# Kernel optimization log

Measured on AMD Instinct MI355X. Metric: run time of the kernel, lower is better.

The kernel has to match this reference:

```python
import jax, jax.numpy as jnp
import numpy as np

S, T, B = 32, 64, 64          # sentences, tokens/sentence, batch
V, E, H, G, C = 32000, 128, 128, 128, 5  # vocab, embed, intra hid, inter hid, classes


def _gru_dir(x, h0, Wih, Whh, bih, bhh):
    # x: [T,B,D]; Wih: [3H,D]; Whh: [3H,H]  (PyTorch GRU gate order r,z,n)
    xg = jnp.einsum('tbd,gd->tbg', x, Wih) + bih  # precompute input gates [T,B,3H]
    def step(h, xt):
        gh = h @ Whh.T + bhh
        ir, iz, inn = jnp.split(xt, 3, axis=-1)
        hr, hz, hn = jnp.split(gh, 3, axis=-1)
        r = jax.nn.sigmoid(ir + hr)
        z = jax.nn.sigmoid(iz + hz)
        n = jnp.tanh(inn + r * hn)
        hnew = (1 - z) * n + z * h
        return hnew, hnew
    _, out = jax.lax.scan(step, h0, xg)
    return out  # [T,B,H]


def _bigru(x, Wih, Whh, bih, bhh):
    # x: [T,B,D]; Wih: [2,3H,D] (fwd, bwd). Zero initial state (init_hidden()).
    h0 = jnp.zeros((x.shape[1], Whh.shape[-1]), x.dtype)
    of = _gru_dir(x, h0, Wih[0], Whh[0], bih[0], bhh[0])
    ob = _gru_dir(x[::-1], h0, Wih[1], Whh[1], bih[1], bhh[1])[::-1]
    return jnp.concatenate([of, ob], axis=-1)  # [T,B,2H]


def setup_inputs() -> dict:
    key = jax.random.key(0)
    ks = iter(jax.random.split(key, 20))
    u = lambda k, shp, s: jax.random.uniform(k, shp, jnp.float32, -s, s)
    tokens = jax.random.randint(next(ks), (S, T, B), 0, V)
    return {
        'tokens': tokens,
        'embed_table': jax.random.normal(next(ks), (V, E), jnp.float32),
        # intra biGRU (input E, hidden H)
        'Wih_intra': u(next(ks), (2, 3 * H, E), 0.08),
        'Whh_intra': u(next(ks), (2, 3 * H, H), 0.08),
        'bih_intra': u(next(ks), (2, 3 * H), 0.08),
        'bhh_intra': u(next(ks), (2, 3 * H), 0.08),
        # intra attention
        'W_W_intra': u(next(ks), (2 * H, 2 * H), 0.1),
        'b_intra': u(next(ks), (2 * H,), 0.1),
        'proj_intra': u(next(ks), (2 * H,), 0.1),
        # inter biGRU (input 2H, hidden G)
        'Wih_inter': u(next(ks), (2, 3 * G, 2 * H), 0.08),
        'Whh_inter': u(next(ks), (2, 3 * G, G), 0.08),
        'bih_inter': u(next(ks), (2, 3 * G), 0.08),
        'bhh_inter': u(next(ks), (2, 3 * G), 0.08),
        # inter attention
        'W_W_inter': u(next(ks), (2 * G, 2 * G), 0.1),
        'b_inter': u(next(ks), (2 * G,), 0.1),
        'proj_inter': u(next(ks), (2 * G,), 0.1),
        # final linear
        'W_final': u(next(ks), (C, 2 * G), 0.06),
        'b_final': u(next(ks), (C,), 0.06),
    }


def reference(tokens, embed_table, Wih_intra, Whh_intra, bih_intra, bhh_intra,
              W_W_intra, b_intra, proj_intra, Wih_inter, Whh_inter, bih_inter,
              bhh_inter, W_W_inter, b_inter, proj_inter, W_final, b_final):
    # ---- intra (word-level) per sentence, fresh zero state each sentence ----
    emb = embed_table[tokens]                                   # [S,T,B,E]
    intra_out = jax.vmap(
        lambda xs: _bigru(xs, Wih_intra, Whh_intra, bih_intra, bhh_intra)
    )(emb)                                                      # [S,T,B,2H]
    u1 = jnp.tanh(jnp.einsum('stbh,hk->stbk', intra_out, W_W_intra) + b_intra)
    a1 = jnp.einsum('stbk,k->stb', u1, proj_intra)              # [S,T,B]
    a1 = jax.nn.softmax(a1, axis=1)                             # softmax over tokens
    sent_vecs = jnp.einsum('stb,stbh->sbh', a1, intra_out)      # [S,B,2H]
    # ---- inter (sentence-level) ----
    inter_out = _bigru(sent_vecs, Wih_inter, Whh_inter, bih_inter, bhh_inter)  # [S,B,2G]
    u2 = jnp.tanh(jnp.einsum('sbh,hk->sbk', inter_out, W_W_inter) + b_inter)
    a2 = jnp.einsum('sbk,k->sb', u2, proj_inter)                # NO softmax (faithful to source)
    doc_vec = jnp.einsum('sb,sbh->bh', a2, inter_out)           # [B,2G]
    final_map = doc_vec @ W_final.T + b_final                   # [B,C]
    return final_map
```

## Files before the change

kernel.cpp:

```cpp
#include <hip/hip_runtime.h>

#define S_ 32
#define T_ 64
#define B_ 64
#define V_ 32000
#define E_ 128
#define H_ 128
#define G_ 128
#define C_ 5

typedef short s8v __attribute__((ext_vector_type(8)));
typedef __bf16 b8v __attribute__((ext_vector_type(8)));
typedef float f32x4 __attribute__((ext_vector_type(4)));

template <typename V>
__device__ inline auto mfma_sel(V a, V b, f32x4 c, int)
    -> decltype(__builtin_amdgcn_mfma_f32_16x16x32_bf16(a, b, c, 0, 0, 0)) {
  return __builtin_amdgcn_mfma_f32_16x16x32_bf16(a, b, c, 0, 0, 0);
}
template <typename V>
__device__ inline f32x4 mfma_sel(V a, V b, f32x4 c, long) {
  return __builtin_amdgcn_mfma_f32_16x16x32_bf16(
      __builtin_bit_cast(b8v, a), __builtin_bit_cast(b8v, b), c, 0, 0, 0);
}
__device__ inline f32x4 mfma16(s8v a, s8v b, f32x4 c) { return mfma_sel(a, b, c, 0); }

__device__ inline float b2f(unsigned short u) {
  union { unsigned int i; float f; } v; v.i = ((unsigned int)u) << 16; return v.f;
}
__device__ inline unsigned short f2b(float f) {
  union { float f; unsigned int i; } v; v.f = f;
  return (unsigned short)((v.i + 0x8000u) >> 16);
}
__device__ inline unsigned short f2b_rne(float f) {
  union { float f; unsigned int i; } v; v.f = f;
  unsigned int r = (v.i + 0x7fffu + ((v.i >> 16) & 1u)) >> 16;
  return (unsigned short)r;
}
__device__ inline s8v cvt8(const float* p) {
  const float4 a = *(const float4*)p;
  const float4 b = *(const float4*)(p + 4);
  s8v r;
  r[0] = (short)f2b_rne(a.x); r[1] = (short)f2b_rne(a.y);
  r[2] = (short)f2b_rne(a.z); r[3] = (short)f2b_rne(a.w);
  r[4] = (short)f2b_rne(b.x); r[5] = (short)f2b_rne(b.y);
  r[6] = (short)f2b_rne(b.z); r[7] = (short)f2b_rne(b.w);
  return r;
}
__device__ inline float fsigm(float x) {
  return __builtin_amdgcn_rcpf(1.f + __builtin_amdgcn_exp2f(-1.44269504f * x));
}
__device__ inline float ftanh(float x) {
  return 1.f - 2.f * __builtin_amdgcn_rcpf(1.f + __builtin_amdgcn_exp2f(2.88539008f * x));
}

__device__ inline void lds_barrier() {
  asm volatile("s_waitcnt lgkmcnt(0)\n\ts_barrier" ::: "memory");
}

__global__ __launch_bounds__(256) void k_gtab(
    const float* __restrict__ emb,
    const float* __restrict__ wih,
    const float* __restrict__ bih,
    const float* __restrict__ bhh,
    const float* __restrict__ wwi,
    unsigned short* __restrict__ gtab,
    unsigned short* __restrict__ wta)
{
  __shared__ __align__(16) unsigned short smem[64 * 264];
  const int bid = blockIdx.x, tid = threadIdx.x;
  if (bid >= 500) {
    const int n0 = (bid - 500) * 64;
    for (int i = 0; i < 64; ++i) {
      int cid = i * 256 + tid;
      int k = cid >> 6, nl = cid & 63;
      smem[nl * 264 + k] = f2b_rne(wwi[k * 256 + n0 + nl]);
    }
    __syncthreads();
    for (int i = 0; i < 8; ++i) {
      int cid = i * 256 + tid;
      int nl = cid >> 5, k8 = cid & 31;
      *(int4*)&wta[(size_t)(n0 + nl) * 256 + k8 * 8] =
          *(const int4*)&smem[nl * 264 + k8 * 8];
    }
    return;
  }
  const int vbase = bid * 64;
  for (int i = 0; i < 8; ++i) {
    int cid = i * 256 + tid;
    int row = cid >> 5, kc = cid & 31;
    float4 v = *(const float4*)&emb[(size_t)(vbase + row) * 128 + kc * 4];
    ushort4 u;
    u.x = f2b_rne(v.x); u.y = f2b_rne(v.y); u.z = f2b_rne(v.z); u.w = f2b_rne(v.w);
    *(ushort4*)&smem[row * 136 + kc * 4] = u;
  }
  __syncthreads();
  const int w = tid >> 6, l = tid & 63, q = l >> 4, ln = l & 15;
  s8v af[4][4];
  for (int mt = 0; mt < 4; ++mt)
    for (int kf = 0; kf < 4; ++kf)
      af[mt][kf] = *(const s8v*)&smem[(mt * 16 + ln) * 136 + kf * 32 + q * 8];
  for (int nchunk = 0; nchunk < 6; ++nchunk) {
    const int nbase = nchunk * 128;
    s8v bf[2][4];
    float bias[2];
    for (int nt = 0; nt < 2; ++nt) {
      int c = nbase + (w * 2 + nt) * 16 + ln;
      int g = (c < 384) ? c : (c - 384);
      bias[nt] = bih[c] + (g < 256 ? bhh[c] : 0.f);
      for (int kf = 0; kf < 4; ++kf)
        bf[nt][kf] = cvt8(&wih[(size_t)c * 128 + kf * 32 + q * 8]);
    }
    for (int mt = 0; mt < 4; ++mt) {
      for (int nt = 0; nt < 2; ++nt) {
        f32x4 acc = {0.f, 0.f, 0.f, 0.f};
        for (int kf = 0; kf < 4; ++kf) acc = mfma16(af[mt][kf], bf[nt][kf], acc);
        const int col = nbase + (w * 2 + nt) * 16 + ln;
        for (int r = 0; r < 4; ++r) {
          const int row = vbase + mt * 16 + q * 4 + r;
          gtab[(size_t)row * 768 + col] = f2b_rne(acc[r] + bias[nt]);
        }
      }
    }
  }
}

__global__ __launch_bounds__(512) void k_intra(
    const int* __restrict__ tokens,
    const unsigned short* __restrict__ gtab,
    const float* __restrict__ whh,
    const float* __restrict__ bhh,
    unsigned short* __restrict__ iout)
{
  const int bid = blockIdx.x;
  const int s = bid >> 3, dir = (bid >> 2) & 1, bq = bid & 3;
  const int bbase = bq * 16;
  const int tid = threadIdx.x;
  const int w = tid >> 6, l = tid & 63, q = l >> 4, ln = l & 15;
  const int gbase = w * 16, g0 = gbase + q * 4;

  __shared__ __align__(16) unsigned short hb[2][16 * 136];
  __shared__ int tokl[T_ * 16];

  for (int i = tid; i < 2 * 16 * 136; i += 512) ((unsigned short*)hb)[i] = 0;
  for (int i = tid; i < T_ * 16; i += 512) {
    int t = i >> 4, bl = i & 15;
    tokl[i] = tokens[(s * T_ + t) * B_ + bbase + bl];
  }

  s8v af[3][4];
  float hbn[4];
  const float* whd = whh + (size_t)dir * (384 * 128);
  const float* bhd = bhh + dir * 384;
  for (int g3 = 0; g3 < 3; ++g3) {
    const int R = g3 * 128 + gbase;
    for (int kf = 0; kf < 4; ++kf)
      af[g3][kf] = cvt8(&whd[(size_t)(R + ln) * 128 + kf * 32 + q * 8]);
  }
  for (int r = 0; r < 4; ++r) hbn[r] = bhd[256 + gbase + q * 4 + r];
  float h[4] = {0.f, 0.f, 0.f, 0.f};
  const int b = bbase + ln;
  __syncthreads();

  ushort4 Xr[4], Xz[4], Xn[4];
#define GLOAD_I(slot, st)                                                   \
  do {                                                                      \
    int tt_ = (st) > (T_ - 1) ? (T_ - 1) : (st);                            \
    int tg_ = dir ? (T_ - 1 - tt_) : tt_;                                   \
    const unsigned short* gp_ =                                             \
        gtab + (size_t)tokl[tg_ * 16 + ln] * 768 + dir * 384 + g0;          \
    Xr[slot] = *(const ushort4*)&gp_[0];                                    \
    Xz[slot] = *(const ushort4*)&gp_[128];                                  \
    Xn[slot] = *(const ushort4*)&gp_[256];                                  \
  } while (0)

  GLOAD_I(0, 0);
  GLOAD_I(1, 1);

  int p = 0;
  for (int it = 0; it < T_ / 4; ++it) {
#pragma unroll
    for (int j = 0; j < 4; ++j) {
      const int step = it * 4 + j;
      const int t = dir ? (T_ - 1 - step) : step;
      GLOAD_I((j + 2) & 3, step + 2);

      s8v bfr[4];
      for (int kf = 0; kf < 4; ++kf)
        bfr[kf] = *(const s8v*)&hb[p][ln * 136 + kf * 32 + q * 8];
      f32x4 c0 = {0.f, 0.f, 0.f, 0.f}, c1 = c0, c2 = c0;
      for (int kf = 0; kf < 4; ++kf) {
        c0 = mfma16(af[0][kf], bfr[kf], c0);
        c1 = mfma16(af[1][kf], bfr[kf], c1);
        c2 = mfma16(af[2][kf], bfr[kf], c2);
      }

      const unsigned short* xrp = (const unsigned short*)&Xr[j];
      const unsigned short* xzp = (const unsigned short*)&Xz[j];
      const unsigned short* xnp = (const unsigned short*)&Xn[j];
      unsigned short hnb[4];
      for (int r = 0; r < 4; ++r) {
        float rr = fsigm(b2f(xrp[r]) + c0[r]);
        float zz = fsigm(b2f(xzp[r]) + c1[r]);
        float nn = ftanh(b2f(xnp[r]) + rr * (c2[r] + hbn[r]));
        float hv = zz * (h[r] - nn) + nn;
        h[r] = hv;
        hnb[r] = f2b(hv);
      }
      ushort4 hv4; hv4.x = hnb[0]; hv4.y = hnb[1]; hv4.z = hnb[2]; hv4.w = hnb[3];
      *(ushort4*)&hb[p ^ 1][ln * 136 + g0] = hv4;
      *(ushort4*)&iout[((size_t)(s * T_ + t) * B_ + b) * 256 + dir * 128 + g0] = hv4;
      lds_barrier();
      p ^= 1;
    }
  }
#undef GLOAD_I
}

__global__ __launch_bounds__(512, 1) void k_attn(
    const unsigned short* __restrict__ iout,
    const unsigned short* __restrict__ wta,
    const float* __restrict__ bint,
    const float* __restrict__ proj,
    float* __restrict__ sv)
{
  __shared__ __align__(16) unsigned short wlds[256 * 256];
  __shared__ float lgbuf[8][16];
  __shared__ float lbuf[8][8];
  const int tid = threadIdx.x, bid = blockIdx.x;
  const int s = bid >> 3, b0 = (bid & 7) * 8;
  for (int i = 0; i < 16; ++i) {
    int cid = i * 512 + tid;
    int n = cid >> 5, kc = cid & 31;
    *(int4*)&wlds[n * 256 + ((kc ^ (n & 15)) << 3)] =
        *(const int4*)&wta[(size_t)n * 256 + kc * 8];
  }
  const int w = tid >> 6, l = tid & 63, q = l >> 4, ln = l & 15;
  float bbv[16], ppv[16];
  for (int nt = 0; nt < 16; ++nt) {
    bbv[nt] = bint[nt * 16 + ln];
    ppv[nt] = proj[nt * 16 + ln];
  }
  __syncthreads();

  float O[8][8];
  for (int kf = 0; kf < 8; ++kf)
    for (int j = 0; j < 8; ++j) O[kf][j] = 0.f;
  float l_acc = 0.f;

  for (int tile = 0; tile < 4; ++tile) {
    const int t = (w * 4 + tile) * 2 + (ln >> 3);
    const size_t row = (size_t)((s * T_ + t) * B_ + b0 + (ln & 7));
    s8v af[8];
    for (int kf = 0; kf < 8; ++kf)
      af[kf] = *(const s8v*)&iout[row * 256 + kf * 32 + q * 8];
    float p0 = 0.f, p1 = 0.f, p2 = 0.f, p3 = 0.f;
    for (int nt = 0; nt < 16; ++nt) {
      f32x4 c = {0.f, 0.f, 0.f, 0.f};
      for (int kf = 0; kf < 8; ++kf) {
        s8v bf = *(const s8v*)&wlds[(nt * 16 + ln) * 256 + (((kf * 4 + q) ^ ln) << 3)];
        c = mfma16(af[kf], bf, c);
      }
      p0 += ppv[nt] * ftanh(c[0] + bbv[nt]);
      p1 += ppv[nt] * ftanh(c[1] + bbv[nt]);
      p2 += ppv[nt] * ftanh(c[2] + bbv[nt]);
      p3 += ppv[nt] * ftanh(c[3] + bbv[nt]);
    }
    for (int d = 1; d < 16; d <<= 1) {
      p0 += __shfl_xor(p0, d); p1 += __shfl_xor(p1, d);
      p2 += __shfl_xor(p2, d); p3 += __shfl_xor(p3, d);
    }
    if (ln == 0) {
      lgbuf[w][q * 4 + 0] = p0; lgbuf[w][q * 4 + 1] = p1;
      lgbuf[w][q * 4 + 2] = p2; lgbuf[w][q * 4 + 3] = p3;
    }
    const float lg = lgbuf[w][ln];
    const float e = __builtin_amdgcn_exp2f(1.44269504f * lg);
    l_acc += e;
    for (int kf = 0; kf < 8; ++kf)
      for (int j = 0; j < 8; ++j)
        O[kf][j] += e * b2f((unsigned short)af[kf][j]);
  }
  l_acc += __shfl_xor(l_acc, 8);
  for (int kf = 0; kf < 8; ++kf)
    for (int j = 0; j < 8; ++j) O[kf][j] += __shfl_xor(O[kf][j], 8);
  __syncthreads();
  float* obuf = (float*)wlds;
  if (ln < 8) {
    const int base = w * 2048 + ln * 256 + q * 8;
    for (int kf = 0; kf < 8; ++kf) {
      float4 v0; v0.x = O[kf][0]; v0.y = O[kf][1]; v0.z = O[kf][2]; v0.w = O[kf][3];
      float4 v1; v1.x = O[kf][4]; v1.y = O[kf][5]; v1.z = O[kf][6]; v1.w = O[kf][7];
      *(float4*)&obuf[base + kf * 32]     = v0;
      *(float4*)&obuf[base + kf * 32 + 4] = v1;
    }
    if (q == 0) lbuf[w][ln] = l_acc;
  }
  __syncthreads();
  const int idx = tid * 4;
  const int bb_ = idx >> 8;
  float4 acc; acc.x = 0.f; acc.y = 0.f; acc.z = 0.f; acc.w = 0.f;
  float lsum = 0.f;
  for (int w8 = 0; w8 < 8; ++w8) {
    const float4 v = *(const float4*)&obuf[w8 * 2048 + idx];
    acc.x += v.x; acc.y += v.y; acc.z += v.z; acc.w += v.w;
    lsum += lbuf[w8][bb_];
  }
  const float inv = __builtin_amdgcn_rcpf(lsum);
  float4 r; r.x = acc.x * inv; r.y = acc.y * inv; r.z = acc.z * inv; r.w = acc.w * inv;
  *(float4*)&sv[(size_t)((s * B_ + b0 + bb_) * 256) + (idx & 255)] = r;
}

__global__ __launch_bounds__(256) void k_xgi(
    const float* __restrict__ sv,
    const float* __restrict__ wihI,
    const float* __restrict__ bihI,
    const float* __restrict__ bhhI,
    float* __restrict__ xgi)
{
  const int bid = blockIdx.x, tid = threadIdx.x;
  const int r0 = bid * 8;
  __shared__ float svl[8 * 256];
  for (int i = 0; i < 8; ++i) svl[i * 256 + tid] = sv[(size_t)(r0 + i) * 256 + tid];
  __syncthreads();
  for (int cc = 0; cc < 3; ++cc) {
    const int c = cc * 256 + tid;
    const int dir = c / 384, g = c - dir * 384;
    const float bias = bihI[c] + (g < 256 ? bhhI[c] : 0.f);
    float acc[8];
    for (int i = 0; i < 8; ++i) acc[i] = bias;
    const float* wr = wihI + (size_t)c * 256;
    for (int hh = 0; hh < 256; ++hh) {
      const float wv = wr[hh];
      for (int i = 0; i < 8; ++i) acc[i] += wv * svl[i * 256 + hh];
    }
    for (int i = 0; i < 8; ++i)
      xgi[((size_t)dir * 2048 + r0 + i) * 384 + g] = acc[i];
  }
}

__global__ __launch_bounds__(512) void k_inter(
    const float* __restrict__ xgi,
    const float* __restrict__ whh,
    const float* __restrict__ bhh,
    float* __restrict__ io2)
{
  const int bid = blockIdx.x;
  const int dir = bid >> 2, bq = bid & 3, bbase = bq * 16;
  const int tid = threadIdx.x;
  const int w = tid >> 6, l = tid & 63, q = l >> 4, ln = l & 15;
  const int gbase = w * 16, g0 = gbase + q * 4;
  __shared__ __align__(16) unsigned short hb[2][16 * 136];
  for (int i = tid; i < 2 * 16 * 136; i += 512) ((unsigned short*)hb)[i] = 0;
  s8v af[3][4];
  float hbn[4];
  const float* whd = whh + (size_t)dir * (384 * 128);
  const float* bhd = bhh + dir * 384;
  for (int g3 = 0; g3 < 3; ++g3) {
    const int R = g3 * 128 + gbase;
    for (int kf = 0; kf < 4; ++kf)
      af[g3][kf] = cvt8(&whd[(size_t)(R + ln) * 128 + kf * 32 + q * 8]);
  }
  for (int r = 0; r < 4; ++r) hbn[r] = bhd[256 + gbase + q * 4 + r];
  float h[4] = {0.f, 0.f, 0.f, 0.f};
  const int b = bbase + ln;
  __syncthreads();

  float4 Vr[4], Vz[4], Vn[4];
#define GLOAD_S(slot, st)                                                   \
  do {                                                                      \
    int tt_ = (st) > (S_ - 1) ? (S_ - 1) : (st);                            \
    int sg_ = dir ? (S_ - 1 - tt_) : tt_;                                   \
    const float* xp_ = xgi + ((size_t)dir * 2048 + sg_ * 64 + b) * 384 + g0;\
    Vr[slot] = *(const float4*)&xp_[0];                                     \
    Vz[slot] = *(const float4*)&xp_[128];                                   \
    Vn[slot] = *(const float4*)&xp_[256];                                   \
  } while (0)

  GLOAD_S(0, 0);
  GLOAD_S(1, 1);

  int p = 0;
  for (int it = 0; it < S_ / 4; ++it) {
#pragma unroll
    for (int j = 0; j < 4; ++j) {
      const int step = it * 4 + j;
      const int sI = dir ? (S_ - 1 - step) : step;
      GLOAD_S((j + 2) & 3, step + 2);

      s8v bfr[4];
      for (int kf = 0; kf < 4; ++kf)
        bfr[kf] = *(const s8v*)&hb[p][ln * 136 + kf * 32 + q * 8];
      f32x4 c0 = {0.f, 0.f, 0.f, 0.f}, c1 = c0, c2 = c0;
      for (int kf = 0; kf < 4; ++kf) {
        c0 = mfma16(af[0][kf], bfr[kf], c0);
        c1 = mfma16(af[1][kf], bfr[kf], c1);
        c2 = mfma16(af[2][kf], bfr[kf], c2);
      }
      const float irv[4] = {Vr[j].x, Vr[j].y, Vr[j].z, Vr[j].w};
      const float izv[4] = {Vz[j].x, Vz[j].y, Vz[j].z, Vz[j].w};
      const float inv[4] = {Vn[j].x, Vn[j].y, Vn[j].z, Vn[j].w};
      unsigned short hnb[4];
      for (int r = 0; r < 4; ++r) {
        float rr = fsigm(irv[r] + c0[r]);
        float zz = fsigm(izv[r] + c1[r]);
        float nn = ftanh(inv[r] + rr * (c2[r] + hbn[r]));
        float hv = zz * (h[r] - nn) + nn;
        h[r] = hv;
        hnb[r] = f2b(hv);
      }
      ushort4 hv4; hv4.x = hnb[0]; hv4.y = hnb[1]; hv4.z = hnb[2]; hv4.w = hnb[3];
      *(ushort4*)&hb[p ^ 1][ln * 136 + g0] = hv4;
      float4 of4; of4.x = h[0]; of4.y = h[1]; of4.z = h[2]; of4.w = h[3];
      *(float4*)&io2[((size_t)(sI * 64 + b)) * 256 + dir * 128 + g0] = of4;
      lds_barrier();
      p ^= 1;
    }
  }
#undef GLOAD_S
}

__global__ __launch_bounds__(256) void k_attn_i(
    const float* __restrict__ io2,
    const float* __restrict__ wwI,
    const float* __restrict__ bI,
    const float* __restrict__ projI,
    float* __restrict__ a2)
{
  const int bid = blockIdx.x, tid = threadIdx.x;
  const int r0 = bid * 8;
  __shared__ float iol[8 * 256];
  __shared__ float red[4 * 8];
  for (int i = 0; i < 8; ++i) iol[i * 256 + tid] = io2[(size_t)(r0 + i) * 256 + tid];
  __syncthreads();
  float acc[8];
  for (int i = 0; i < 8; ++i) acc[i] = 0.f;
  for (int hh = 0; hh < 256; ++hh) {
    const float wv = wwI[hh * 256 + tid];
    for (int i = 0; i < 8; ++i) acc[i] += wv * iol[i * 256 + hh];
  }
  const float bb = bI[tid], pp = projI[tid];
  float p[8];
  for (int i = 0; i < 8; ++i) p[i] = pp * ftanh(acc[i] + bb);
  for (int d = 1; d < 64; d <<= 1)
    for (int i = 0; i < 8; ++i) p[i] += __shfl_xor(p[i], d);
  const int w = tid >> 6, l = tid & 63;
  if (l == 0)
    for (int i = 0; i < 8; ++i) red[w * 8 + i] = p[i];
  __syncthreads();
  if (tid < 8) a2[r0 + tid] = red[tid] + red[8 + tid] + red[16 + tid] + red[24 + tid];
}

__global__ __launch_bounds__(256) void k_final(
    const float* __restrict__ a2,
    const float* __restrict__ io2,
    const float* __restrict__ wf,
    const float* __restrict__ bfi,
    float* __restrict__ out)
{
  const int b = blockIdx.x, tid = threadIdx.x;
  __shared__ float av[S_];
  __shared__ float dv[256];
  __shared__ float red[4];
  if (tid < S_) av[tid] = a2[tid * 64 + b];
  __syncthreads();
  float acc = 0.f;
  for (int s = 0; s < S_; ++s) acc += av[s] * io2[((size_t)(s * 64 + b)) * 256 + tid];
  dv[tid] = acc;
  __syncthreads();
  for (int c = 0; c < C_; ++c) {
    float pv = wf[c * 256 + tid] * dv[tid];
    for (int d = 1; d < 64; d <<= 1) pv += __shfl_xor(pv, d);
    const int w = tid >> 6, l = tid & 63;
    if (l == 0) red[w] = pv;
    __syncthreads();
    if (tid == 0)
      out[b * C_ + c] = red[0] + red[1] + red[2] + red[3] + bfi[c];
    __syncthreads();
  }
}

extern "C" void kernel_launch(void* const* d_in, const int* in_sizes, int n_in,
                              void* d_out, int out_size, void* d_ws, size_t ws_size,
                              hipStream_t stream) {
  (void)in_sizes; (void)n_in; (void)out_size; (void)ws_size;
  const int*   tokens = (const int*)d_in[0];
  const float* emb    = (const float*)d_in[1];
  const float* wih_a  = (const float*)d_in[2];
  const float* whh_a  = (const float*)d_in[3];
  const float* bih_a  = (const float*)d_in[4];
  const float* bhh_a  = (const float*)d_in[5];
  const float* ww_a   = (const float*)d_in[6];
  const float* b_a    = (const float*)d_in[7];
  const float* proj_a = (const float*)d_in[8];
  const float* wih_i  = (const float*)d_in[9];
  const float* whh_i  = (const float*)d_in[10];
  const float* bih_i  = (const float*)d_in[11];
  const float* bhh_i  = (const float*)d_in[12];
  const float* ww_i   = (const float*)d_in[13];
  const float* b_i    = (const float*)d_in[14];
  const float* proj_i = (const float*)d_in[15];
  const float* w_fin  = (const float*)d_in[16];
  const float* b_fin  = (const float*)d_in[17];

  char* ws = (char*)d_ws;
  unsigned short* gtab = (unsigned short*)(ws + 0);
  unsigned short* wta  = (unsigned short*)(ws + 49152000);
  unsigned short* iout = (unsigned short*)(ws + 49283072);
  float* sv  = (float*)(ws + 117440512);
  float* xgi = (float*)(ws + 119537664);
  float* io2 = (float*)(ws + 125829120);
  float* a2  = (float*)(ws + 127926272);

  k_gtab<<<504, 256, 0, stream>>>(emb, wih_a, bih_a, bhh_a, ww_a, gtab, wta);
  k_intra<<<256, 512, 0, stream>>>(tokens, gtab, whh_a, bhh_a, iout);
  k_attn<<<256, 512, 0, stream>>>(iout, wta, b_a, proj_a, sv);
  k_xgi<<<256, 256, 0, stream>>>(sv, wih_i, bih_i, bhh_i, xgi);
  k_inter<<<8, 512, 0, stream>>>(xgi, whh_i, bhh_i, io2);
  k_attn_i<<<256, 256, 0, stream>>>(io2, ww_i, b_i, proj_i, a2);
  k_final<<<64, 256, 0, stream>>>(a2, io2, w_fin, b_fin, (float*)d_out);
}
```

Before: 311.8 us.

## Fuse inter-GRU input projection into intra attention via bf16 MFMA, deepen prefetch

Removes the separate k_xgi kernel. The intra attention kernel now writes its sentence vectors as bf16 to LDS and computes the inter-GRU input gate projection there with MFMA, using a bf16 copy of Wih_inter that k_gtab now also produces. This drops one launch, the fp32 sv round trip through global memory and the scalar FMA GEMM, at the cost of bf16 rounding on the sentence vectors and the weights. The token row offset is also precomputed in LDS, and the GRU gate prefetch distance goes from two steps to three in both recurrent kernels, which adds register pressure.

```diff
diff --git a/kernel.cpp b/kernel.cpp
--- a/kernel.cpp
+++ b/kernel.cpp
@@ -64,11 +64,24 @@
     const float* __restrict__ bih,
     const float* __restrict__ bhh,
     const float* __restrict__ wwi,
+    const float* __restrict__ wihI,
     unsigned short* __restrict__ gtab,
-    unsigned short* __restrict__ wta)
+    unsigned short* __restrict__ wta,
+    unsigned short* __restrict__ wib)
 {
   __shared__ __align__(16) unsigned short smem[64 * 264];
   const int bid = blockIdx.x, tid = threadIdx.x;
+  if (bid >= 504) {
+    const int cb = bid - 504;
+    for (int i = 0; i < 48; ++i) {
+      int e4 = cb * 12288 + i * 256 + tid;
+      float4 v = *(const float4*)&wihI[(size_t)e4 * 4];
+      ushort4 u;
+      u.x = f2b_rne(v.x); u.y = f2b_rne(v.y); u.z = f2b_rne(v.z); u.w = f2b_rne(v.w);
+      *(ushort4*)&wib[(size_t)e4 * 4] = u;
+    }
+    return;
+  }
   if (bid >= 500) {
     const int n0 = (bid - 500) * 64;
     for (int i = 0; i < 64; ++i) {
@@ -145,7 +158,7 @@
   for (int i = tid; i < 2 * 16 * 136; i += 512) ((unsigned short*)hb)[i] = 0;
   for (int i = tid; i < T_ * 16; i += 512) {
     int t = i >> 4, bl = i & 15;
-    tokl[i] = tokens[(s * T_ + t) * B_ + bbase + bl];
+    tokl[i] = tokens[(s * T_ + t) * B_ + bbase + bl] * 768 + dir * 384;
   }
 
   s8v af[3][4];
@@ -168,7 +181,7 @@
     int tt_ = (st) > (T_ - 1) ? (T_ - 1) : (st);                            \
     int tg_ = dir ? (T_ - 1 - tt_) : tt_;                                   \
     const unsigned short* gp_ =                                             \
-        gtab + (size_t)tokl[tg_ * 16 + ln] * 768 + dir * 384 + g0;          \
+        gtab + (size_t)(tokl[tg_ * 16 + ln] + g0);                          \
     Xr[slot] = *(const ushort4*)&gp_[0];                                    \
     Xz[slot] = *(const ushort4*)&gp_[128];                                  \
     Xn[slot] = *(const ushort4*)&gp_[256];                                  \
@@ -176,6 +189,7 @@
 
   GLOAD_I(0, 0);
   GLOAD_I(1, 1);
+  GLOAD_I(2, 2);
 
   int p = 0;
   for (int it = 0; it < T_ / 4; ++it) {
@@ -183,7 +197,7 @@
     for (int j = 0; j < 4; ++j) {
       const int step = it * 4 + j;
       const int t = dir ? (T_ - 1 - step) : step;
-      GLOAD_I((j + 2) & 3, step + 2);
+      GLOAD_I((j + 3) & 3, step + 3);
 
       s8v bfr[4];
       for (int kf = 0; kf < 4; ++kf)
@@ -222,7 +236,10 @@
     const unsigned short* __restrict__ wta,
     const float* __restrict__ bint,
     const float* __restrict__ proj,
-    float* __restrict__ sv)
+    const unsigned short* __restrict__ wib,
+    const float* __restrict__ bihI,
+    const float* __restrict__ bhhI,
+    float* __restrict__ xgi)
 {
   __shared__ __align__(16) unsigned short wlds[256 * 256];
   __shared__ float lgbuf[8][16];
@@ -286,6 +303,7 @@
     for (int j = 0; j < 8; ++j) O[kf][j] += __shfl_xor(O[kf][j], 8);
   __syncthreads();
   float* obuf = (float*)wlds;
+  unsigned short* svl = (unsigned short*)(((char*)wlds) + 65536);
   if (ln < 8) {
     const int base = w * 2048 + ln * 256 + q * 8;
     for (int kf = 0; kf < 8; ++kf) {
@@ -295,6 +313,11 @@
       *(float4*)&obuf[base + kf * 32 + 4] = v1;
     }
     if (q == 0) lbuf[w][ln] = l_acc;
+  }
+  {
+    ushort4 z4; z4.x = 0; z4.y = 0; z4.z = 0; z4.w = 0;
+    int rr = 8 + (tid >> 6), cc = (tid & 63) * 4;
+    *(ushort4*)&svl[rr * 264 + cc] = z4;
   }
   __syncthreads();
   const int idx = tid * 4;
@@ -307,35 +330,30 @@
     lsum += lbuf[w8][bb_];
   }
   const float inv = __builtin_amdgcn_rcpf(lsum);
-  float4 r; r.x = acc.x * inv; r.y = acc.y * inv; r.z = acc.z * inv; r.w = acc.w * inv;
-  *(float4*)&sv[(size_t)((s * B_ + b0 + bb_) * 256) + (idx & 255)] = r;
-}
-
-__global__ __launch_bounds__(256) void k_xgi(
-    const float* __restrict__ sv,
-    const float* __restrict__ wihI,
-    const float* __restrict__ bihI,
-    const float* __restrict__ bhhI,
-    float* __restrict__ xgi)
-{
-  const int bid = blockIdx.x, tid = threadIdx.x;
-  const int r0 = bid * 8;
-  __shared__ float svl[8 * 256];
-  for (int i = 0; i < 8; ++i) svl[i * 256 + tid] = sv[(size_t)(r0 + i) * 256 + tid];
-  __syncthreads();
-  for (int cc = 0; cc < 3; ++cc) {
-    const int c = cc * 256 + tid;
-    const int dir = c / 384, g = c - dir * 384;
-    const float bias = bihI[c] + (g < 256 ? bhhI[c] : 0.f);
-    float acc[8];
-    for (int i = 0; i < 8; ++i) acc[i] = bias;
-    const float* wr = wihI + (size_t)c * 256;
-    for (int hh = 0; hh < 256; ++hh) {
-      const float wv = wr[hh];
-      for (int i = 0; i < 8; ++i) acc[i] += wv * svl[i * 256 + hh];
-    }
-    for (int i = 0; i < 8; ++i)
-      xgi[((size_t)dir * 2048 + r0 + i) * 384 + g] = acc[i];
+  ushort4 u;
+  u.x = f2b_rne(acc.x * inv); u.y = f2b_rne(acc.y * inv);
+  u.z = f2b_rne(acc.z * inv); u.w = f2b_rne(acc.w * inv);
+  *(ushort4*)&svl[bb_ * 264 + (idx & 255)] = u;
+  __syncthreads();
+  s8v afx[8];
+  for (int kf = 0; kf < 8; ++kf)
+    afx[kf] = *(const s8v*)&svl[ln * 264 + kf * 32 + q * 8];
+  for (int nt = 0; nt < 6; ++nt) {
+    const int c = w * 96 + nt * 16 + ln;
+    const int dirI = (c >= 384) ? 1 : 0;
+    const int g = c - dirI * 384;
+    const float biasx = bihI[c] + (g < 256 ? bhhI[c] : 0.f);
+    f32x4 cacc = {0.f, 0.f, 0.f, 0.f};
+    for (int kf = 0; kf < 8; ++kf) {
+      s8v bfx = *(const s8v*)&wib[(size_t)c * 256 + kf * 32 + q * 8];
+      cacc = mfma16(afx[kf], bfx, cacc);
+    }
+    if (q < 2) {
+      for (int r = 0; r < 4; ++r) {
+        const int m = q * 4 + r;
+        xgi[((size_t)dirI * 2048 + s * B_ + b0 + m) * 384 + g] = cacc[r] + biasx;
+      }
+    }
   }
 }
 
@@ -379,6 +397,7 @@
 
   GLOAD_S(0, 0);
   GLOAD_S(1, 1);
+  GLOAD_S(2, 2);
 
   int p = 0;
   for (int it = 0; it < S_ / 4; ++it) {
@@ -386,7 +405,7 @@
     for (int j = 0; j < 4; ++j) {
       const int step = it * 4 + j;
       const int sI = dir ? (S_ - 1 - step) : step;
-      GLOAD_S((j + 2) & 3, step + 2);
+      GLOAD_S((j + 3) & 3, step + 3);
 
       s8v bfr[4];
       for (int kf = 0; kf < 4; ++kf)
@@ -507,15 +526,15 @@
   unsigned short* gtab = (unsigned short*)(ws + 0);
   unsigned short* wta  = (unsigned short*)(ws + 49152000);
   unsigned short* iout = (unsigned short*)(ws + 49283072);
-  float* sv  = (float*)(ws + 117440512);
+  unsigned short* wib  = (unsigned short*)(ws + 116391936);
   float* xgi = (float*)(ws + 119537664);
   float* io2 = (float*)(ws + 125829120);
   float* a2  = (float*)(ws + 127926272);
 
-  k_gtab<<<504, 256, 0, stream>>>(emb, wih_a, bih_a, bhh_a, ww_a, gtab, wta);
+  k_gtab<<<508, 256, 0, stream>>>(emb, wih_a, bih_a, bhh_a, ww_a, wih_i,
+                                  gtab, wta, wib);
   k_intra<<<256, 512, 0, stream>>>(tokens, gtab, whh_a, bhh_a, iout);
-  k_attn<<<256, 512, 0, stream>>>(iout, wta, b_a, proj_a, sv);
-  k_xgi<<<256, 256, 0, stream>>>(sv, wih_i, bih_i, bhh_i, xgi);
+  k_attn<<<256, 512, 0, stream>>>(iout, wta, b_a, proj_a, wib, bih_i, bhh_i, xgi);
   k_inter<<<8, 512, 0, stream>>>(xgi, whh_i, bhh_i, io2);
   k_attn_i<<<256, 256, 0, stream>>>(io2, ww_i, b_i, proj_i, a2);
   k_final<<<64, 256, 0, stream>>>(a2, io2, w_fin, b_fin, (float*)d_out);
```

After: 289.6 us. 7.1% less time.
